# Kernel tuning notes

Measured on AMD Instinct MI355X. Metric: run time of the kernel, lower is better.

The kernel has to match this reference:

```python
import jax, jax.numpy as jnp
import numpy as np

N_NODES = 100000
K_NBRS = 16
N_EDGES = N_NODES * K_NBRS


def setup_inputs() -> dict:
    key = jax.random.key(0)
    ks = jax.random.split(key, 20)
    x = jax.random.normal(ks[0], (N_NODES, 3), dtype=jnp.float32)
    # knn-like edge list: every node is the target of exactly K_NBRS edges
    dst = jnp.repeat(jnp.arange(N_NODES, dtype=jnp.int64), K_NBRS)
    src = jax.random.randint(ks[1], (N_EDGES,), 0, N_NODES, dtype=jnp.int64)
    edge_index = jnp.stack([src, dst], axis=0)  # [2, E], row0=source(j), row1=target(i)

    def lin_init(k, fan_in, fan_out):
        s = 1.0 / np.sqrt(fan_in)
        return jax.random.uniform(k, (fan_in, fan_out), jnp.float32, -s, s)

    inp = {"x": x, "edge_index": edge_index}
    inp["W1"], inp["b1"] = lin_init(ks[2], 6, 64), jnp.zeros((64,), jnp.float32)
    for i, kk in zip(range(2, 6), ks[3:7]):
        inp[f"W{i}"] = lin_init(kk, 128, 64)
        inp[f"b{i}"] = jnp.zeros((64,), jnp.float32)
    inp["Wa"], inp["ba"] = lin_init(ks[8], 128, 128), jnp.zeros((128,), jnp.float32)
    inp["Wb"], inp["bb"] = lin_init(ks[9], 128, 3), jnp.zeros((3,), jnp.float32)
    return inp


def edge_conv(x, src, dst, W, b):
    # PyG EdgeConv: message = nn(cat([x_i, x_j - x_i])), max-aggregate at target i
    xi = x[dst]                      # [E, C] center (target) features
    xj = x[src]                      # [E, C] neighbor (source) features
    msg = jnp.concatenate([xi, xj - xi], axis=-1)  # [E, 2C]
    msg = jax.nn.relu(msg @ W + b)                 # [E, 64] per-edge MLP
    return jax.ops.segment_max(msg, dst, num_segments=N_NODES)  # [N, 64]


def reference(x, edge_index, W1, b1, W2, b2, W3, b3, W4, b4, W5, b5, Wa, ba, Wb, bb):
    src, dst = edge_index[0], edge_index[1]
    h = edge_conv(x, src, dst, W1, b1)
    h = edge_conv(h, src, dst, W2, b2)
    h = edge_conv(h, src, dst, W3, b3)
    h = edge_conv(h, src, dst, W4, b4)
    h = edge_conv(h, src, dst, W5, b5)           # [N, 64]
    g = jnp.max(h, axis=0, keepdims=True)        # [1, 64] global max
    feat = jnp.concatenate([h, jnp.broadcast_to(g, h.shape)], axis=1)  # [N, 128]
    out = jax.nn.relu(feat @ Wa + ba) @ Wb + bb  # [N, 3]
    return x + out
```

## Files before the change

### kernel.cpp

```cpp
#include <hip/hip_runtime.h>
#include <math.h>

#define N_NODES 100000
#define K_NBRS 16
#define N_EDGES (N_NODES * K_NBRS)
#define TPB 256
#define NBLK 2048

typedef __attribute__((ext_vector_type(8))) short short8;
typedef __attribute__((ext_vector_type(4))) float float4_;
typedef __attribute__((ext_vector_type(4))) int int4_;
typedef __attribute__((ext_vector_type(4))) unsigned short ushort4_;

__device__ __forceinline__ unsigned short f2bf(float f) {
  unsigned int u = __float_as_uint(f);
  u += 0x7fffu + ((u >> 16) & 1u);
  return (unsigned short)(u >> 16);
}
__device__ __forceinline__ float bf2f(unsigned short b) {
  return __uint_as_float(((unsigned int)b) << 16);
}

__global__ void k_pre(const int* __restrict__ ei, int* __restrict__ srcout,
                      const float* __restrict__ x, const float* __restrict__ W1,
                      const float* __restrict__ b1,
                      unsigned short* __restrict__ A, unsigned short* __restrict__ B) {
  const bool is64 = (ei[1] == 0) && (ei[3] == 0) && (ei[5] == 0) && (ei[7] == 0);
  const int tid = blockIdx.x * blockDim.x + threadIdx.x;
  const int stride = gridDim.x * blockDim.x;
  for (int e = tid; e < N_EDGES; e += stride)
    srcout[e] = is64 ? ei[2 * e] : ei[e];

  const int lane = threadIdx.x & 63;
  const int nwaves = stride >> 6;
  const int wid0 = tid >> 6;
  float w[6];
#pragma unroll
  for (int k = 0; k < 6; ++k) w[k] = W1[k * 64 + lane];
  const float bias = b1[lane];
  for (int i0 = wid0; i0 < N_NODES; i0 += nwaves) {
    const int i = __builtin_amdgcn_readfirstlane(i0);
    const float x0 = x[3 * i], x1 = x[3 * i + 1], x2 = x[3 * i + 2];
    const float b = fmaf(x0, w[3], fmaf(x1, w[4], x2 * w[5]));
    const float a = bias + fmaf(x0, w[0] - w[3],
                          fmaf(x1, w[1] - w[4], x2 * (w[2] - w[5])));
    A[(size_t)i * 64 + lane] = f2bf(a);
    B[(size_t)i * 64 + lane] = f2bf(b);
  }
}

template <bool DO_GMAX>
__global__ void k_aggr(const int* __restrict__ src,
                       const unsigned short* __restrict__ Ain,
                       const unsigned short* __restrict__ Bin,
                       unsigned short* __restrict__ hout, float* __restrict__ P) {
  const int lane = threadIdx.x & 63;
  const int q = lane >> 4;
  const int c4 = (lane & 15) * 4;
  const int nw = (gridDim.x * blockDim.x) >> 6;
  const int w0 = (blockIdx.x * blockDim.x + threadIdx.x) >> 6;
  float4_ gmax = (float4_)(0.f);
  int p = w0;
  int4_ idx[4];
  ushort4_ avp;
  if (p * 4 < N_NODES) {
    const int i0 = __builtin_amdgcn_readfirstlane(p * 4);
#pragma unroll
    for (int n = 0; n < 4; ++n)
      idx[n] = *(const int4_*)(src + (size_t)(i0 + n) * 16 + q * 4);
    avp = *(const ushort4_*)(Ain + (size_t)(i0 + q) * 64 + c4);
  }
  while (p * 4 < N_NODES) {
    const int i0 = __builtin_amdgcn_readfirstlane(p * 4);
    ushort4_ gv[4][4];
#pragma unroll
    for (int n = 0; n < 4; ++n)
#pragma unroll
      for (int e = 0; e < 4; ++e)
        gv[n][e] = *(const ushort4_*)(Bin + (size_t)idx[n][e] * 64 + c4);
    const int pn = p + nw;
    int4_ idxn[4];
    ushort4_ avn;
    if (pn * 4 < N_NODES) {
      const int i1 = __builtin_amdgcn_readfirstlane(pn * 4);
#pragma unroll
      for (int n = 0; n < 4; ++n)
        idxn[n] = *(const int4_*)(src + (size_t)(i1 + n) * 16 + q * 4);
      avn = *(const ushort4_*)(Ain + (size_t)(i1 + q) * 64 + c4);
    }
    float4_ m[4];
#pragma unroll
    for (int n = 0; n < 4; ++n) {
#pragma unroll
      for (int t = 0; t < 4; ++t) {
        const float v0 = bf2f(gv[n][0][t]), v1 = bf2f(gv[n][1][t]);
        const float v2 = bf2f(gv[n][2][t]), v3 = bf2f(gv[n][3][t]);
        m[n][t] = fmaxf(fmaxf(v0, v1), fmaxf(v2, v3));
      }
#pragma unroll
      for (int t = 0; t < 4; ++t) {
        float v = m[n][t];
        v = fmaxf(v, __shfl_xor(v, 16));
        v = fmaxf(v, __shfl_xor(v, 32));
        m[n][t] = v;
      }
    }
    ushort4_ hb;
#pragma unroll
    for (int t = 0; t < 4; ++t) {
      float v = m[0][t];
      v = (q == 1) ? m[1][t] : v;
      v = (q == 2) ? m[2][t] : v;
      v = (q == 3) ? m[3][t] : v;
      const float h = fmaxf(bf2f(avp[t]) + v, 0.f);
      hb[t] = f2bf(h);
      if constexpr (DO_GMAX) gmax[t] = fmaxf(gmax[t], h);
    }
    *(ushort4_*)(hout + (size_t)(i0 + q) * 64 + c4) = hb;
    p = pn;
#pragma unroll
    for (int n = 0; n < 4; ++n) idx[n] = idxn[n];
    avp = avn;
  }
  if constexpr (DO_GMAX) {
    __shared__ float red[TPB][4];
#pragma unroll
    for (int t = 0; t < 4; ++t) red[threadIdx.x][t] = gmax[t];
    __syncthreads();
    if (threadIdx.x < 64) {
      const int c = threadIdx.x, j = c >> 2, t = c & 3;
      float mm = 0.f;
#pragma unroll
      for (int w = 0; w < 4; ++w)
#pragma unroll
        for (int qq = 0; qq < 4; ++qq)
          mm = fmaxf(mm, red[w * 64 + qq * 16 + j][t]);
      P[(size_t)blockIdx.x * 64 + c] = mm;
    }
  }
}

__global__ __launch_bounds__(TPB, 2)
void k_gemm(const unsigned short* __restrict__ h, const float* __restrict__ W,
            const float* __restrict__ bn,
            unsigned short* __restrict__ Aout, unsigned short* __restrict__ Bout) {
  __shared__ unsigned short lwhi[128 * 72];
  __shared__ unsigned short lwlo[128 * 72];
  for (int idx = threadIdx.x; idx < 8192; idx += TPB) {
    const int k = idx >> 7, j = idx & 127;
    const float v = (j < 64) ? (W[k * 64 + j] - W[(64 + k) * 64 + j])
                             : W[(64 + k) * 64 + (j - 64)];
    const unsigned short hi = f2bf(v);
    lwhi[j * 72 + k] = hi;
    lwlo[j * 72 + k] = f2bf(v - bf2f(hi));
  }
  __syncthreads();
  const int lane = threadIdx.x & 63;
  const int wav = threadIdx.x >> 6;
  const int l15 = lane & 15, lg = lane >> 4;
  short8 bhi[8][2], blo[8][2];
#pragma unroll
  for (int ct = 0; ct < 8; ++ct)
#pragma unroll
    for (int kk = 0; kk < 2; ++kk) {
      const int off = (ct * 16 + l15) * 72 + kk * 32 + lg * 8;
      bhi[ct][kk] = *(const short8*)&lwhi[off];
      blo[ct][kk] = *(const short8*)&lwlo[off];
    }
  float bv[4];
#pragma unroll
  for (int ct = 0; ct < 4; ++ct) bv[ct] = bn[ct * 16 + l15];
  const int NT = (N_NODES + 63) / 64;
  for (int t = blockIdx.x; t < NT; t += gridDim.x) {
    const int nb = t * 64 + wav * 16;
    const int row = min(nb + l15, N_NODES - 1);
    const unsigned short* hr = h + (size_t)row * 64;
    float4_ acc[8];
#pragma unroll
    for (int ct = 0; ct < 8; ++ct) acc[ct] = (float4_)(0.f);
#pragma unroll
    for (int kk = 0; kk < 2; ++kk) {
      const short8 ahi = *(const short8*)(hr + kk * 32 + lg * 8);
#pragma unroll
      for (int ct = 0; ct < 8; ++ct) {
        acc[ct] = __builtin_amdgcn_mfma_f32_16x16x32_bf16(ahi, bhi[ct][kk], acc[ct], 0, 0, 0);
        acc[ct] = __builtin_amdgcn_mfma_f32_16x16x32_bf16(ahi, blo[ct][kk], acc[ct], 0, 0, 0);
      }
    }
#pragma unroll
    for (int ct = 0; ct < 8; ++ct)
#pragma unroll
      for (int r = 0; r < 4; ++r) {
        const int node = nb + lg * 4 + r;
        if (node < N_NODES) {
          if (ct < 4)
            Aout[(size_t)node * 64 + ct * 16 + l15] = f2bf(acc[ct][r] + bv[ct]);
          else
            Bout[(size_t)node * 64 + (ct - 4) * 16 + l15] = f2bf(acc[ct][r]);
        }
      }
  }
}

__global__ void k_gred(const float* __restrict__ P, float* __restrict__ g) {
  __shared__ float red[16][64];
  const int lane = threadIdx.x & 63;
  const int w = threadIdx.x >> 6;
  float m = 0.f;
  for (int r = w; r < NBLK; r += 16)
    m = fmaxf(m, P[(size_t)r * 64 + lane]);
  red[w][lane] = m;
  __syncthreads();
  if (threadIdx.x < 64) {
    float mm = 0.f;
#pragma unroll
    for (int k = 0; k < 16; ++k) mm = fmaxf(mm, red[k][lane]);
    g[lane] = mm;
  }
}

__global__ __launch_bounds__(TPB, 2)
void k_final(const unsigned short* __restrict__ h, const float* __restrict__ g,
             const float* __restrict__ Wa, const float* __restrict__ ba,
             const float* __restrict__ Wb, const float* __restrict__ bb,
             const float* __restrict__ x, float* __restrict__ out) {
  __shared__ unsigned short lwhi[128 * 72];
  __shared__ unsigned short lwlo[128 * 72];
  __shared__ float sgt[128];
  for (int idx = threadIdx.x; idx < 8192; idx += TPB) {
    const int k = idx >> 7, j = idx & 127;
    const float v = Wa[k * 128 + j];
    const unsigned short hi = f2bf(v);
    lwhi[j * 72 + k] = hi;
    lwlo[j * 72 + k] = f2bf(v - bf2f(hi));
  }
  if (threadIdx.x < 128) {
    const int c = threadIdx.x;
    float s = ba[c];
    for (int k = 0; k < 64; ++k) s = fmaf(g[k], Wa[(64 + k) * 128 + c], s);
    sgt[c] = s;
  }
  __syncthreads();
  const int lane = threadIdx.x & 63;
  const int wav = threadIdx.x >> 6;
  const int l15 = lane & 15, lg = lane >> 4;
  short8 bhi[8][2], blo[8][2];
#pragma unroll
  for (int ct = 0; ct < 8; ++ct)
#pragma unroll
    for (int kk = 0; kk < 2; ++kk) {
      const int off = (ct * 16 + l15) * 72 + kk * 32 + lg * 8;
      bhi[ct][kk] = *(const short8*)&lwhi[off];
      blo[ct][kk] = *(const short8*)&lwlo[off];
    }
  float gtv[8];
#pragma unroll
  for (int ct = 0; ct < 8; ++ct) gtv[ct] = sgt[ct * 16 + l15];
  float wbv[8][3];
#pragma unroll
  for (int ct = 0; ct < 8; ++ct)
#pragma unroll
    for (int jj = 0; jj < 3; ++jj)
      wbv[ct][jj] = Wb[(ct * 16 + l15) * 3 + jj];
  const float bbl = (l15 == 0) ? bb[0] : (l15 == 1 ? bb[1] : bb[2]);
  const int NT = (N_NODES + 63) / 64;
  for (int t = blockIdx.x; t < NT; t += gridDim.x) {
    const int nb = t * 64 + wav * 16;
    const int row = min(nb + l15, N_NODES - 1);
    const unsigned short* hr = h + (size_t)row * 64;
    float4_ acc[8];
#pragma unroll
    for (int ct = 0; ct < 8; ++ct) acc[ct] = (float4_)(0.f);
#pragma unroll
    for (int kk = 0; kk < 2; ++kk) {
      const short8 ahi = *(const short8*)(hr + kk * 32 + lg * 8);
#pragma unroll
      for (int ct = 0; ct < 8; ++ct) {
        acc[ct] = __builtin_amdgcn_mfma_f32_16x16x32_bf16(ahi, bhi[ct][kk], acc[ct], 0, 0, 0);
        acc[ct] = __builtin_amdgcn_mfma_f32_16x16x32_bf16(ahi, blo[ct][kk], acc[ct], 0, 0, 0);
      }
    }
#pragma unroll
    for (int r = 0; r < 4; ++r) {
      float t0 = 0.f, t1 = 0.f, t2 = 0.f;
#pragma unroll
      for (int ct = 0; ct < 8; ++ct) {
        const float hd = fmaxf(acc[ct][r] + gtv[ct], 0.f);
        t0 = fmaf(hd, wbv[ct][0], t0);
        t1 = fmaf(hd, wbv[ct][1], t1);
        t2 = fmaf(hd, wbv[ct][2], t2);
      }
#pragma unroll
      for (int off = 1; off < 16; off <<= 1) {
        t0 += __shfl_xor(t0, off);
        t1 += __shfl_xor(t1, off);
        t2 += __shfl_xor(t2, off);
      }
      const int node = nb + lg * 4 + r;
      if (node < N_NODES && l15 < 3) {
        const float tj = (l15 == 0) ? t0 : (l15 == 1 ? t1 : t2);
        out[(size_t)node * 3 + l15] = x[(size_t)node * 3 + l15] + tj + bbl;
      }
    }
  }
}

extern "C" void kernel_launch(void* const* d_in, const int* in_sizes, int n_in,
                              void* d_out, int out_size, void* d_ws, size_t ws_size,
                              hipStream_t stream) {
  const float* x  = (const float*)d_in[0];
  const int*   ei = (const int*)d_in[1];
  const float* W1 = (const float*)d_in[2];
  const float* b1 = (const float*)d_in[3];
  const float* W2 = (const float*)d_in[4];
  const float* b2 = (const float*)d_in[5];
  const float* W3 = (const float*)d_in[6];
  const float* b3 = (const float*)d_in[7];
  const float* W4 = (const float*)d_in[8];
  const float* b4 = (const float*)d_in[9];
  const float* W5 = (const float*)d_in[10];
  const float* b5 = (const float*)d_in[11];
  const float* Wa = (const float*)d_in[12];
  const float* ba = (const float*)d_in[13];
  const float* Wb = (const float*)d_in[14];
  const float* bb = (const float*)d_in[15];
  float* out = (float*)d_out;

  float* ws = (float*)d_ws;
  int* srcbuf = (int*)ws;
  unsigned short* A0 = (unsigned short*)(ws + 1600000);
  unsigned short* A1 = A0 + 6400000;
  unsigned short* H  = A1 + 6400000;
  unsigned short* B0 = H + 6400000;
  unsigned short* B1 = B0 + 6400000;
  float* P = (float*)(B1 + 6400000);
  float* g = P + (size_t)NBLK * 64;

  k_pre<<<NBLK, TPB, 0, stream>>>(ei, srcbuf, x, W1, b1, A0, B0);
  k_aggr<false><<<NBLK, TPB, 0, stream>>>(srcbuf, A0, B0, H, nullptr);
  k_gemm<<<1024, TPB, 0, stream>>>(H, W2, b2, A1, B1);
  k_aggr<false><<<NBLK, TPB, 0, stream>>>(srcbuf, A1, B1, H, nullptr);
  k_gemm<<<1024, TPB, 0, stream>>>(H, W3, b3, A0, B0);
  k_aggr<false><<<NBLK, TPB, 0, stream>>>(srcbuf, A0, B0, H, nullptr);
  k_gemm<<<1024, TPB, 0, stream>>>(H, W4, b4, A1, B1);
  k_aggr<false><<<NBLK, TPB, 0, stream>>>(srcbuf, A1, B1, H, nullptr);
  k_gemm<<<1024, TPB, 0, stream>>>(H, W5, b5, A0, B0);
  k_aggr<true><<<NBLK, TPB, 0, stream>>>(srcbuf, A0, B0, H, P);
  k_gred<<<1, 1024, 0, stream>>>(P, g);
  k_final<<<1024, TPB, 0, stream>>>(H, g, Wa, ba, Wb, bb, x, out);
}
```

Before: 400.2 us.

## Fuse edge max-aggregation with next layer's GEMM via shared-memory tile

Merges the per-layer aggregation and weight GEMM into one kernel: each block aggregates 16 nodes into an LDS tile, then runs MFMA on it to produce the next layer's A/B projections. This removes the H round trip through global memory and four kernel launches. In exchange, every block rebuilds the split bf16 weights in LDS, uses two block barriers per 16-node tile, and drops the software prefetch of neighbour indices. The final kernel grid is also halved.

```diff
diff --git a/kernel.cpp b/kernel.cpp
--- a/kernel.cpp
+++ b/kernel.cpp
@@ -6,6 +6,7 @@
 #define N_EDGES (N_NODES * K_NBRS)
 #define TPB 256
 #define NBLK 2048
+#define NTILES (N_NODES / 16)
 
 typedef __attribute__((ext_vector_type(8))) short short8;
 typedef __attribute__((ext_vector_type(4))) float float4_;
@@ -49,103 +50,15 @@
   }
 }
 
-template <bool DO_GMAX>
-__global__ void k_aggr(const int* __restrict__ src,
-                       const unsigned short* __restrict__ Ain,
-                       const unsigned short* __restrict__ Bin,
-                       unsigned short* __restrict__ hout, float* __restrict__ P) {
-  const int lane = threadIdx.x & 63;
-  const int q = lane >> 4;
-  const int c4 = (lane & 15) * 4;
-  const int nw = (gridDim.x * blockDim.x) >> 6;
-  const int w0 = (blockIdx.x * blockDim.x + threadIdx.x) >> 6;
-  float4_ gmax = (float4_)(0.f);
-  int p = w0;
-  int4_ idx[4];
-  ushort4_ avp;
-  if (p * 4 < N_NODES) {
-    const int i0 = __builtin_amdgcn_readfirstlane(p * 4);
-#pragma unroll
-    for (int n = 0; n < 4; ++n)
-      idx[n] = *(const int4_*)(src + (size_t)(i0 + n) * 16 + q * 4);
-    avp = *(const ushort4_*)(Ain + (size_t)(i0 + q) * 64 + c4);
-  }
-  while (p * 4 < N_NODES) {
-    const int i0 = __builtin_amdgcn_readfirstlane(p * 4);
-    ushort4_ gv[4][4];
-#pragma unroll
-    for (int n = 0; n < 4; ++n)
-#pragma unroll
-      for (int e = 0; e < 4; ++e)
-        gv[n][e] = *(const ushort4_*)(Bin + (size_t)idx[n][e] * 64 + c4);
-    const int pn = p + nw;
-    int4_ idxn[4];
-    ushort4_ avn;
-    if (pn * 4 < N_NODES) {
-      const int i1 = __builtin_amdgcn_readfirstlane(pn * 4);
-#pragma unroll
-      for (int n = 0; n < 4; ++n)
-        idxn[n] = *(const int4_*)(src + (size_t)(i1 + n) * 16 + q * 4);
-      avn = *(const ushort4_*)(Ain + (size_t)(i1 + q) * 64 + c4);
-    }
-    float4_ m[4];
-#pragma unroll
-    for (int n = 0; n < 4; ++n) {
-#pragma unroll
-      for (int t = 0; t < 4; ++t) {
-        const float v0 = bf2f(gv[n][0][t]), v1 = bf2f(gv[n][1][t]);
-        const float v2 = bf2f(gv[n][2][t]), v3 = bf2f(gv[n][3][t]);
-        m[n][t] = fmaxf(fmaxf(v0, v1), fmaxf(v2, v3));
-      }
-#pragma unroll
-      for (int t = 0; t < 4; ++t) {
-        float v = m[n][t];
-        v = fmaxf(v, __shfl_xor(v, 16));
-        v = fmaxf(v, __shfl_xor(v, 32));
-        m[n][t] = v;
-      }
-    }
-    ushort4_ hb;
-#pragma unroll
-    for (int t = 0; t < 4; ++t) {
-      float v = m[0][t];
-      v = (q == 1) ? m[1][t] : v;
-      v = (q == 2) ? m[2][t] : v;
-      v = (q == 3) ? m[3][t] : v;
-      const float h = fmaxf(bf2f(avp[t]) + v, 0.f);
-      hb[t] = f2bf(h);
-      if constexpr (DO_GMAX) gmax[t] = fmaxf(gmax[t], h);
-    }
-    *(ushort4_*)(hout + (size_t)(i0 + q) * 64 + c4) = hb;
-    p = pn;
-#pragma unroll
-    for (int n = 0; n < 4; ++n) idx[n] = idxn[n];
-    avp = avn;
-  }
-  if constexpr (DO_GMAX) {
-    __shared__ float red[TPB][4];
-#pragma unroll
-    for (int t = 0; t < 4; ++t) red[threadIdx.x][t] = gmax[t];
-    __syncthreads();
-    if (threadIdx.x < 64) {
-      const int c = threadIdx.x, j = c >> 2, t = c & 3;
-      float mm = 0.f;
-#pragma unroll
-      for (int w = 0; w < 4; ++w)
-#pragma unroll
-        for (int qq = 0; qq < 4; ++qq)
-          mm = fmaxf(mm, red[w * 64 + qq * 16 + j][t]);
-      P[(size_t)blockIdx.x * 64 + c] = mm;
-    }
-  }
-}
-
-__global__ __launch_bounds__(TPB, 2)
-void k_gemm(const unsigned short* __restrict__ h, const float* __restrict__ W,
-            const float* __restrict__ bn,
-            unsigned short* __restrict__ Aout, unsigned short* __restrict__ Bout) {
-  __shared__ unsigned short lwhi[128 * 72];
-  __shared__ unsigned short lwlo[128 * 72];
+__global__ __launch_bounds__(TPB, 4)
+void k_fused(const int* __restrict__ src,
+             const unsigned short* __restrict__ Ain,
+             const unsigned short* __restrict__ Bin,
+             const float* __restrict__ W, const float* __restrict__ bn,
+             unsigned short* __restrict__ Aout, unsigned short* __restrict__ Bout) {
+  __shared__ __align__(16) unsigned short lwhi[128 * 72];
+  __shared__ __align__(16) unsigned short lwlo[128 * 72];
+  __shared__ __align__(16) unsigned short lh[16 * 72];
   for (int idx = threadIdx.x; idx < 8192; idx += TPB) {
     const int k = idx >> 7, j = idx & 127;
     const float v = (j < 64) ? (W[k * 64 + j] - W[(64 + k) * 64 + j])
@@ -154,51 +67,156 @@
     lwhi[j * 72 + k] = hi;
     lwlo[j * 72 + k] = f2bf(v - bf2f(hi));
   }
+  const int lane = threadIdx.x & 63;
+  const int wav = threadIdx.x >> 6;
+  const int q = lane >> 4;
+  const int l15 = lane & 15;
+  const int c4 = l15 * 4;
+  float bv0 = 0.f, bv1 = 0.f;
+  if (wav < 2) {
+    bv0 = bn[(2 * wav) * 16 + l15];
+    bv1 = bn[(2 * wav + 1) * 16 + l15];
+  }
   __syncthreads();
-  const int lane = threadIdx.x & 63;
-  const int wav = threadIdx.x >> 6;
-  const int l15 = lane & 15, lg = lane >> 4;
-  short8 bhi[8][2], blo[8][2];
-#pragma unroll
-  for (int ct = 0; ct < 8; ++ct)
-#pragma unroll
-    for (int kk = 0; kk < 2; ++kk) {
-      const int off = (ct * 16 + l15) * 72 + kk * 32 + lg * 8;
-      bhi[ct][kk] = *(const short8*)&lwhi[off];
-      blo[ct][kk] = *(const short8*)&lwlo[off];
-    }
-  float bv[4];
-#pragma unroll
-  for (int ct = 0; ct < 4; ++ct) bv[ct] = bn[ct * 16 + l15];
-  const int NT = (N_NODES + 63) / 64;
-  for (int t = blockIdx.x; t < NT; t += gridDim.x) {
-    const int nb = t * 64 + wav * 16;
-    const int row = min(nb + l15, N_NODES - 1);
-    const unsigned short* hr = h + (size_t)row * 64;
-    float4_ acc[8];
-#pragma unroll
-    for (int ct = 0; ct < 8; ++ct) acc[ct] = (float4_)(0.f);
-#pragma unroll
-    for (int kk = 0; kk < 2; ++kk) {
-      const short8 ahi = *(const short8*)(hr + kk * 32 + lg * 8);
-#pragma unroll
-      for (int ct = 0; ct < 8; ++ct) {
-        acc[ct] = __builtin_amdgcn_mfma_f32_16x16x32_bf16(ahi, bhi[ct][kk], acc[ct], 0, 0, 0);
-        acc[ct] = __builtin_amdgcn_mfma_f32_16x16x32_bf16(ahi, blo[ct][kk], acc[ct], 0, 0, 0);
-      }
-    }
-#pragma unroll
-    for (int ct = 0; ct < 8; ++ct)
-#pragma unroll
-      for (int r = 0; r < 4; ++r) {
-        const int node = nb + lg * 4 + r;
-        if (node < N_NODES) {
-          if (ct < 4)
-            Aout[(size_t)node * 64 + ct * 16 + l15] = f2bf(acc[ct][r] + bv[ct]);
-          else
-            Bout[(size_t)node * 64 + (ct - 4) * 16 + l15] = f2bf(acc[ct][r]);
-        }
-      }
+  for (int t = blockIdx.x; t < NTILES; t += gridDim.x) {
+    const int i0 = t * 16 + wav * 4;
+    int4_ idx[4];
+#pragma unroll
+    for (int n = 0; n < 4; ++n)
+      idx[n] = *(const int4_*)(src + (size_t)(i0 + n) * 16 + q * 4);
+    ushort4_ gv[4][4];
+#pragma unroll
+    for (int n = 0; n < 4; ++n)
+#pragma unroll
+      for (int e = 0; e < 4; ++e)
+        gv[n][e] = *(const ushort4_*)(Bin + (size_t)idx[n][e] * 64 + c4);
+    const ushort4_ av = *(const ushort4_*)(Ain + (size_t)(i0 + q) * 64 + c4);
+    float4_ m[4];
+#pragma unroll
+    for (int n = 0; n < 4; ++n) {
+#pragma unroll
+      for (int tt = 0; tt < 4; ++tt) {
+        const float v0 = bf2f(gv[n][0][tt]), v1 = bf2f(gv[n][1][tt]);
+        const float v2 = bf2f(gv[n][2][tt]), v3 = bf2f(gv[n][3][tt]);
+        m[n][tt] = fmaxf(fmaxf(v0, v1), fmaxf(v2, v3));
+      }
+#pragma unroll
+      for (int tt = 0; tt < 4; ++tt) {
+        float v = m[n][tt];
+        v = fmaxf(v, __shfl_xor(v, 16));
+        v = fmaxf(v, __shfl_xor(v, 32));
+        m[n][tt] = v;
+      }
+    }
+    ushort4_ hb;
+#pragma unroll
+    for (int tt = 0; tt < 4; ++tt) {
+      float v = m[0][tt];
+      v = (q == 1) ? m[1][tt] : v;
+      v = (q == 2) ? m[2][tt] : v;
+      v = (q == 3) ? m[3][tt] : v;
+      hb[tt] = f2bf(fmaxf(bf2f(av[tt]) + v, 0.f));
+    }
+    *(ushort4_*)&lh[(wav * 4 + q) * 72 + c4] = hb;
+    __syncthreads();
+    const short8 a0 = *(const short8*)&lh[l15 * 72 + q * 8];
+    const short8 a1 = *(const short8*)&lh[l15 * 72 + 32 + q * 8];
+    float4_ acc0 = (float4_)(0.f), acc1 = (float4_)(0.f);
+    {
+      const int ct0 = wav * 2, ct1 = wav * 2 + 1;
+      const int r0 = (ct0 * 16 + l15) * 72 + q * 8;
+      const int r1 = (ct1 * 16 + l15) * 72 + q * 8;
+      acc0 = __builtin_amdgcn_mfma_f32_16x16x32_bf16(a0, *(const short8*)&lwhi[r0], acc0, 0, 0, 0);
+      acc0 = __builtin_amdgcn_mfma_f32_16x16x32_bf16(a0, *(const short8*)&lwlo[r0], acc0, 0, 0, 0);
+      acc0 = __builtin_amdgcn_mfma_f32_16x16x32_bf16(a1, *(const short8*)&lwhi[r0 + 32], acc0, 0, 0, 0);
+      acc0 = __builtin_amdgcn_mfma_f32_16x16x32_bf16(a1, *(const short8*)&lwlo[r0 + 32], acc0, 0, 0, 0);
+      acc1 = __builtin_amdgcn_mfma_f32_16x16x32_bf16(a0, *(const short8*)&lwhi[r1], acc1, 0, 0, 0);
+      acc1 = __builtin_amdgcn_mfma_f32_16x16x32_bf16(a0, *(const short8*)&lwlo[r1], acc1, 0, 0, 0);
+      acc1 = __builtin_amdgcn_mfma_f32_16x16x32_bf16(a1, *(const short8*)&lwhi[r1 + 32], acc1, 0, 0, 0);
+      acc1 = __builtin_amdgcn_mfma_f32_16x16x32_bf16(a1, *(const short8*)&lwlo[r1 + 32], acc1, 0, 0, 0);
+    }
+#pragma unroll
+    for (int r = 0; r < 4; ++r) {
+      const int node = t * 16 + q * 4 + r;
+      const int ct0 = wav * 2, ct1 = wav * 2 + 1;
+      if (wav < 2) {
+        Aout[(size_t)node * 64 + ct0 * 16 + l15] = f2bf(acc0[r] + bv0);
+        Aout[(size_t)node * 64 + ct1 * 16 + l15] = f2bf(acc1[r] + bv1);
+      } else {
+        Bout[(size_t)node * 64 + (ct0 - 4) * 16 + l15] = f2bf(acc0[r]);
+        Bout[(size_t)node * 64 + (ct1 - 4) * 16 + l15] = f2bf(acc1[r]);
+      }
+    }
+    __syncthreads();
+  }
+}
+
+__global__ void k_aggr_last(const int* __restrict__ src,
+                            const unsigned short* __restrict__ Ain,
+                            const unsigned short* __restrict__ Bin,
+                            unsigned short* __restrict__ hout, float* __restrict__ P) {
+  const int lane = threadIdx.x & 63;
+  const int q = lane >> 4;
+  const int c4 = (lane & 15) * 4;
+  const int nw = (gridDim.x * blockDim.x) >> 6;
+  const int w0 = (blockIdx.x * blockDim.x + threadIdx.x) >> 6;
+  float4_ gmax = (float4_)(0.f);
+  for (int p = w0; p * 4 < N_NODES; p += nw) {
+    const int i0 = __builtin_amdgcn_readfirstlane(p * 4);
+    int4_ idx[4];
+#pragma unroll
+    for (int n = 0; n < 4; ++n)
+      idx[n] = *(const int4_*)(src + (size_t)(i0 + n) * 16 + q * 4);
+    ushort4_ gv[4][4];
+#pragma unroll
+    for (int n = 0; n < 4; ++n)
+#pragma unroll
+      for (int e = 0; e < 4; ++e)
+        gv[n][e] = *(const ushort4_*)(Bin + (size_t)idx[n][e] * 64 + c4);
+    const ushort4_ av = *(const ushort4_*)(Ain + (size_t)(i0 + q) * 64 + c4);
+    float4_ m[4];
+#pragma unroll
+    for (int n = 0; n < 4; ++n) {
+#pragma unroll
+      for (int tt = 0; tt < 4; ++tt) {
+        const float v0 = bf2f(gv[n][0][tt]), v1 = bf2f(gv[n][1][tt]);
+        const float v2 = bf2f(gv[n][2][tt]), v3 = bf2f(gv[n][3][tt]);
+        m[n][tt] = fmaxf(fmaxf(v0, v1), fmaxf(v2, v3));
+      }
+#pragma unroll
+      for (int tt = 0; tt < 4; ++tt) {
+        float v = m[n][tt];
+        v = fmaxf(v, __shfl_xor(v, 16));
+        v = fmaxf(v, __shfl_xor(v, 32));
+        m[n][tt] = v;
+      }
+    }
+    ushort4_ hb;
+#pragma unroll
+    for (int tt = 0; tt < 4; ++tt) {
+      float v = m[0][tt];
+      v = (q == 1) ? m[1][tt] : v;
+      v = (q == 2) ? m[2][tt] : v;
+      v = (q == 3) ? m[3][tt] : v;
+      const float h = fmaxf(bf2f(av[tt]) + v, 0.f);
+      hb[tt] = f2bf(h);
+      gmax[tt] = fmaxf(gmax[tt], h);
+    }
+    *(ushort4_*)(hout + (size_t)(i0 + q) * 64 + c4) = hb;
+  }
+  __shared__ float red[TPB][4];
+#pragma unroll
+  for (int tt = 0; tt < 4; ++tt) red[threadIdx.x][tt] = gmax[tt];
+  __syncthreads();
+  if (threadIdx.x < 64) {
+    const int c = threadIdx.x, j = c >> 2, tt = c & 3;
+    float mm = 0.f;
+#pragma unroll
+    for (int w = 0; w < 4; ++w)
+#pragma unroll
+      for (int qq = 0; qq < 4; ++qq)
+        mm = fmaxf(mm, red[w * 64 + qq * 16 + j][tt]);
+    P[(size_t)blockIdx.x * 64 + c] = mm;
   }
 }
 
@@ -224,8 +242,8 @@
              const float* __restrict__ Wa, const float* __restrict__ ba,
              const float* __restrict__ Wb, const float* __restrict__ bb,
              const float* __restrict__ x, float* __restrict__ out) {
-  __shared__ unsigned short lwhi[128 * 72];
-  __shared__ unsigned short lwlo[128 * 72];
+  __shared__ __align__(16) unsigned short lwhi[128 * 72];
+  __shared__ __align__(16) unsigned short lwlo[128 * 72];
   __shared__ float sgt[128];
   for (int idx = threadIdx.x; idx < 8192; idx += TPB) {
     const int k = idx >> 7, j = idx & 127;
@@ -329,23 +347,19 @@
   float* ws = (float*)d_ws;
   int* srcbuf = (int*)ws;
   unsigned short* A0 = (unsigned short*)(ws + 1600000);
-  unsigned short* A1 = A0 + 6400000;
-  unsigned short* H  = A1 + 6400000;
-  unsigned short* B0 = H + 6400000;
-  unsigned short* B1 = B0 + 6400000;
-  float* P = (float*)(B1 + 6400000);
+  unsigned short* B0 = A0 + 6400000;
+  unsigned short* A1 = B0 + 6400000;
+  unsigned short* B1 = A1 + 6400000;
+  unsigned short* H  = B1 + 6400000;
+  float* P = (float*)(H + 6400000);
   float* g = P + (size_t)NBLK * 64;
 
   k_pre<<<NBLK, TPB, 0, stream>>>(ei, srcbuf, x, W1, b1, A0, B0);
-  k_aggr<false><<<NBLK, TPB, 0, stream>>>(srcbuf, A0, B0, H, nullptr);
-  k_gemm<<<1024, TPB, 0, stream>>>(H, W2, b2, A1, B1);
-  k_aggr<false><<<NBLK, TPB, 0, stream>>>(srcbuf, A1, B1, H, nullptr);
-  k_gemm<<<1024, TPB, 0, stream>>>(H, W3, b3, A0, B0);
-  k_aggr<false><<<NBLK, TPB, 0, stream>>>(srcbuf, A0, B0, H, nullptr);
-  k_gemm<<<1024, TPB, 0, stream>>>(H, W4, b4, A1, B1);
-  k_aggr<false><<<NBLK, TPB, 0, stream>>>(srcbuf, A1, B1, H, nullptr);
-  k_gemm<<<1024, TPB, 0, stream>>>(H, W5, b5, A0, B0);
-  k_aggr<true><<<NBLK, TPB, 0, stream>>>(srcbuf, A0, B0, H, P);
+  k_fused<<<NBLK, TPB, 0, stream>>>(srcbuf, A0, B0, W2, b2, A1, B1);
+  k_fused<<<NBLK, TPB, 0, stream>>>(srcbuf, A1, B1, W3, b3, A0, B0);
+  k_fused<<<NBLK, TPB, 0, stream>>>(srcbuf, A0, B0, W4, b4, A1, B1);
+  k_fused<<<NBLK, TPB, 0, stream>>>(srcbuf, A1, B1, W5, b5, A0, B0);
+  k_aggr_last<<<NBLK, TPB, 0, stream>>>(srcbuf, A0, B0, H, P);
   k_gred<<<1, 1024, 0, stream>>>(P, g);
-  k_final<<<1024, TPB, 0, stream>>>(H, g, Wa, ba, Wb, bb, x, out);
-}
+  k_final<<<512, TPB, 0, stream>>>(H, g, Wa, ba, Wb, bb, x, out);
+}
```

Result: faster. 374.6 us (-6.4%).
